# Optimization experiments

Measured on AMD Instinct MI355X. Metric: run time of the kernel, lower is better.

Reference implementation:

```python
import jax, jax.numpy as jnp
import numpy as np

B = 512        # events (graphs) in batch
NPE = 512      # nodes per event (structured so knn can be batched)
N = B * NPE    # total nodes = 262144
K = 6          # knn neighbors
F_IN = 128     # 2 * n_samples
H = 16         # conv1 out
OUT = 10       # graph_out
COORD_MAX = 16 # detector grid extent


def setup_inputs() -> dict:
    key = jax.random.key(0)
    k1, k2, k3, k4 = jax.random.split(key, 4)
    xy = jax.random.randint(k1, (N, 2), 0, COORD_MAX, dtype=jnp.int32)
    batch = jnp.repeat(jnp.arange(B, dtype=jnp.int32), NPE)  # coo[:,2] = event id
    coo = jnp.concatenate([xy, batch[:, None]], axis=1)       # [N,3] int
    x = jax.random.normal(k2, (N, F_IN), dtype=jnp.float32)
    W1 = jax.random.normal(k3, (F_IN, H), dtype=jnp.float32) * (1.0 / np.sqrt(F_IN))
    b1 = jnp.zeros((H,), dtype=jnp.float32)
    W2 = jax.random.normal(k4, (H, OUT), dtype=jnp.float32) * (1.0 / np.sqrt(H))
    b2 = jnp.zeros((OUT,), dtype=jnp.float32)
    return {"coo": coo, "x": x, "W1": W1, "b1": b1, "W2": W2, "b2": b2}


def knn_edges(coo):
    # knn_graph(coo, K, batch=coo[:,2], loop=False): batches are contiguous
    # blocks of NPE nodes, so reshape and do per-event brute-force knn.
    pos = coo.astype(jnp.float32).reshape(B, NPE, 3)
    # squared pairwise distances per event: [B, n, n]
    d = jnp.sum((pos[:, :, None, :] - pos[:, None, :, :]) ** 2, axis=-1)
    d = d + jnp.eye(NPE, dtype=d.dtype) * 1e9  # exclude self (loop=False)
    _, idx = jax.lax.top_k(-d, K)              # [B, n, K] neighbor indices (local)
    base = (jnp.arange(B, dtype=jnp.int32) * NPE)[:, None, None]
    src = (idx.astype(jnp.int32) + base).reshape(-1)                       # j (neighbor)
    dst = jnp.broadcast_to(jnp.arange(NPE, dtype=jnp.int32)[None, :, None] + base,
                           (B, NPE, K)).reshape(-1)                        # i (center)
    return src, dst


def gcn_conv(x, W, b, src, dst):
    # GCNConv: out = D^{-1/2} (A + I) D^{-1/2} X W + b
    loops = jnp.arange(N, dtype=jnp.int32)
    row = jnp.concatenate([dst, loops])  # target
    col = jnp.concatenate([src, loops])  # source
    deg = jax.ops.segment_sum(jnp.ones_like(row, dtype=x.dtype), row, num_segments=N)
    dinv = jnp.where(deg > 0, jax.lax.rsqrt(deg), 0.0)
    norm = dinv[row] * dinv[col]         # [E]
    h = x @ W                            # [N, F_out]
    msg = h[col] * norm[:, None]         # gather + scale
    return jax.ops.segment_sum(msg, row, num_segments=N) + b


def reference(coo, x, W1, b1, W2, b2):
    src, dst = knn_edges(coo)
    h = jax.nn.relu(gcn_conv(x, W1, b1, src, dst))
    out = gcn_conv(h, W2, b2, src, dst)  # [N, OUT] per-node output (n_lin == 0)
    return out
```

## Files before the change

### kernel.cpp

```cpp
#include <hip/hip_runtime.h>

#define NPE   512
#define F_IN  128
#define HDIM  16
#define ODIM  10

typedef __attribute__((ext_vector_type(8))) short short8;
typedef __attribute__((ext_vector_type(4))) float f32x4;

static __device__ __forceinline__ short f2bf(float f) {
  unsigned u = __builtin_bit_cast(unsigned, f);
  u = (u + 0x7fffu + ((u >> 16) & 1u)) >> 16;
  return (short)u;
}
static __device__ __forceinline__ float bflo(unsigned d) {
  return __builtin_bit_cast(float, d << 16);
}
static __device__ __forceinline__ float bfhi(unsigned d) {
  return __builtin_bit_cast(float, d & 0xffff0000u);
}
static __device__ __forceinline__ unsigned umin2(unsigned a, unsigned b) { return a < b ? a : b; }
static __device__ __forceinline__ unsigned umax2(unsigned a, unsigned b) { return a > b ? a : b; }

__global__ __launch_bounds__(512, 4) void gnet_fused(
    const int* __restrict__ coo, const float* __restrict__ x,
    const float* __restrict__ W1, const float* __restrict__ b1,
    const float* __restrict__ W2, const float* __restrict__ b2,
    float* __restrict__ out)
{
  __shared__ __align__(16) short    hbuf[NPE][24];
  __shared__ __align__(16) short    r_s [NPE][24];
  __shared__ unsigned       cnt_s [256];
  __shared__ unsigned       scan_s[256];
  __shared__ unsigned       cur_s [256];
  __shared__ unsigned       wtot_s[4];
  __shared__ unsigned short bucket_s[NPE];
  __shared__ unsigned       top7_s[256][8];
  __shared__ unsigned       tile_c;

  const int tid   = threadIdx.x;
  const int gbase = blockIdx.x * NPE;
  const int ln    = tid & 63;
  const int wv    = tid >> 6;
  const int lcol  = ln & 15;
  const int lkg   = ln >> 4;

  const int cx = coo[(gbase + tid) * 3 + 0];
  const int cy = coo[(gbase + tid) * 3 + 1];
  const int mycell = cy * 16 + cx;

  if (tid < 256) cnt_s[tid] = 0;
  if (tid == 0)  tile_c = 0;
  __syncthreads();
  atomicAdd(&cnt_s[mycell], 1u);
  __syncthreads();
  unsigned sv = 0;
  if (tid < 256) {
    sv = cnt_s[tid];
#pragma unroll
    for (int off = 1; off < 64; off <<= 1) {
      unsigned u = __shfl_up(sv, off, 64);
      if (ln >= off) sv += u;
    }
    if (ln == 63) wtot_s[wv] = sv;
  }
  __syncthreads();
  if (tid < 256) {
    unsigned add = 0;
#pragma unroll
    for (int w = 0; w < 3; ++w) if (w < wv) add += wtot_s[w];
    sv += add;
    scan_s[tid] = sv;
    cur_s[tid]  = sv - cnt_s[tid];
  }
  __syncthreads();
  {
    const unsigned slot = atomicAdd(&cur_s[mycell], 1u);
    bucket_s[slot] = (unsigned short)tid;
  }
  __syncthreads();

  short8 bw1[4];
#pragma unroll
  for (int s = 0; s < 4; ++s) {
#pragma unroll
    for (int e = 0; e < 8; ++e) {
      const int k = s * 32 + lkg * 8 + e;
      bw1[s][e] = f2bf(W1[k * HDIM + lcol]);
    }
  }

  if (tid < 256 && cnt_s[tid] != 0) {
    const int ccx = tid & 15, ccy = tid >> 4;
    unsigned k0 = 0x7fffffffu, k1 = k0, k2 = k0, k3 = k0, k4 = k0, k5 = k0, k6 = k0;
    auto insert7 = [&](unsigned key) {
      if (key < k6) {
        k6 = key;
        unsigned lo, hi;
        lo = umin2(k5, k6); hi = umax2(k5, k6); k5 = lo; k6 = hi;
        lo = umin2(k4, k5); hi = umax2(k4, k5); k4 = lo; k5 = hi;
        lo = umin2(k3, k4); hi = umax2(k3, k4); k3 = lo; k4 = hi;
        lo = umin2(k2, k3); hi = umax2(k2, k3); k2 = lo; k3 = hi;
        lo = umin2(k1, k2); hi = umax2(k1, k2); k1 = lo; k2 = hi;
        lo = umin2(k0, k1); hi = umax2(k0, k1); k0 = lo; k1 = hi;
      }
    };
    auto scan_cell = [&](int c, unsigned kb) {
      const unsigned e = scan_s[c];
      const unsigned n = cnt_s[c];
      for (unsigned q = e - n; q < e; ++q) insert7(kb | (unsigned)bucket_s[q]);
    };
    scan_cell(tid, 0u);
    for (int r = 1; r <= 15; ++r) {
      const unsigned r2 = (unsigned)(r * r);
      if (r2 > (k6 >> 9)) break;
      for (int sg = 0; sg < 2; ++sg) {
        const int yy = ccy + (sg ? r : -r);
        if (yy < 0 || yy > 15) continue;
        const int xlo = ccx - r < 0 ? 0 : ccx - r;
        const int xhi = ccx + r > 15 ? 15 : ccx + r;
        for (int xx = xlo; xx <= xhi; ++xx) {
          const int dx = xx - ccx;
          const unsigned kb = (unsigned)(dx * dx + (int)r2) << 9;
          if (kb < k6) scan_cell(yy * 16 + xx, kb);
        }
      }
      for (int sg = 0; sg < 2; ++sg) {
        const int xx = ccx + (sg ? r : -r);
        if (xx < 0 || xx > 15) continue;
        const int ylo = ccy - r + 1 < 0 ? 0 : ccy - r + 1;
        const int yhi = ccy + r - 1 > 15 ? 15 : ccy + r - 1;
        for (int yy = ylo; yy <= yhi; ++yy) {
          const int dy = yy - ccy;
          const unsigned kb = (unsigned)(dy * dy + (int)r2) << 9;
          if (kb < k6) scan_cell(yy * 16 + xx, kb);
        }
      }
    }
    unsigned* tp = top7_s[tid];
    tp[0] = k0; tp[1] = k1; tp[2] = k2; tp[3] = k3; tp[4] = k4; tp[5] = k5; tp[6] = k6;
  }

  for (;;) {
    int t = 0;
    if (ln == 0) t = (int)atomicAdd(&tile_c, 1u);
    t = __shfl(t, 0, 64);
    if (t >= 32) break;
    const int nt = t * 16;
    f32x4 acc = {0.f, 0.f, 0.f, 0.f};
#pragma unroll
    for (int s = 0; s < 4; ++s) {
      const float* xp = x + (size_t)(gbase + nt + lcol) * F_IN + s * 32 + lkg * 8;
      const float4 xa = *reinterpret_cast<const float4*>(xp);
      const float4 xb = *reinterpret_cast<const float4*>(xp + 4);
      short8 af;
      af[0] = f2bf(xa.x); af[1] = f2bf(xa.y); af[2] = f2bf(xa.z); af[3] = f2bf(xa.w);
      af[4] = f2bf(xb.x); af[5] = f2bf(xb.y); af[6] = f2bf(xb.z); af[7] = f2bf(xb.w);
      acc = __builtin_amdgcn_mfma_f32_16x16x32_bf16(af, bw1[s], acc, 0, 0, 0);
    }
#pragma unroll
    for (int i = 0; i < 4; ++i) {
      hbuf[nt + lkg * 4 + i][lcol] = f2bf(acc[i]);
    }
  }
  __syncthreads();

  const unsigned* tp = top7_s[mycell];
  const unsigned t0 = tp[0], t1 = tp[1], t2 = tp[2], t3 = tp[3];
  const unsigned t4 = tp[4], t5 = tp[5], t6 = tp[6];
  const unsigned selfkey = (unsigned)tid;
  int p = 7;
  p = (t6 == selfkey) ? 6 : p;
  p = (t5 == selfkey) ? 5 : p;
  p = (t4 == selfkey) ? 4 : p;
  p = (t3 == selfkey) ? 3 : p;
  p = (t2 == selfkey) ? 2 : p;
  p = (t1 == selfkey) ? 1 : p;
  p = (t0 == selfkey) ? 0 : p;
  const int nb0 = (int)((p > 0 ? t0 : t1) & 511u);
  const int nb1 = (int)((p > 1 ? t1 : t2) & 511u);
  const int nb2 = (int)((p > 2 ? t2 : t3) & 511u);
  const int nb3 = (int)((p > 3 ? t3 : t4) & 511u);
  const int nb4 = (int)((p > 4 ? t4 : t5) & 511u);
  const int nb5 = (int)((p > 5 ? t5 : t6) & 511u);

  {
    float acc[HDIM];
#pragma unroll
    for (int o = 0; o < HDIM; ++o) acc[o] = 0.f;
    const int rows[7] = {tid, nb0, nb1, nb2, nb3, nb4, nb5};
#pragma unroll
    for (int r = 0; r < 7; ++r) {
      const unsigned* hp = reinterpret_cast<const unsigned*>(hbuf[rows[r]]);
      const uint4 ha = *reinterpret_cast<const uint4*>(hp);
      const uint4 hb = *reinterpret_cast<const uint4*>(hp + 4);
      const unsigned hd[8] = {ha.x, ha.y, ha.z, ha.w, hb.x, hb.y, hb.z, hb.w};
#pragma unroll
      for (int q = 0; q < 8; ++q) {
        acc[2 * q]     += bflo(hd[q]);
        acc[2 * q + 1] += bfhi(hd[q]);
      }
    }
    const float inv = 1.0f / 7.0f;
    unsigned* rp = reinterpret_cast<unsigned*>(r_s[tid]);
#pragma unroll
    for (int q = 0; q < 8; ++q) {
      const float v0 = fmaxf(acc[2 * q]     * inv + b1[2 * q],     0.f);
      const float v1 = fmaxf(acc[2 * q + 1] * inv + b1[2 * q + 1], 0.f);
      rp[q] = (unsigned)(unsigned short)f2bf(v0) |
              ((unsigned)(unsigned short)f2bf(v1) << 16);
    }
  }
  __syncthreads();

  float* h2f = reinterpret_cast<float*>(hbuf);
  short8 bw2 = {0, 0, 0, 0, 0, 0, 0, 0};
  if (lkg < 2 && lcol < ODIM) {
#pragma unroll
    for (int e = 0; e < 8; ++e) {
      const int k = lkg * 8 + e;
      bw2[e] = f2bf(W2[k * ODIM + lcol]);
    }
  }
#pragma unroll
  for (int t = 0; t < 4; ++t) {
    const int nt = wv * 64 + t * 16;
    short8 af = {0, 0, 0, 0, 0, 0, 0, 0};
    if (lkg < 2) {
      af = *reinterpret_cast<const short8*>(&r_s[nt + lcol][lkg * 8]);
    }
    f32x4 acc = {0.f, 0.f, 0.f, 0.f};
    acc = __builtin_amdgcn_mfma_f32_16x16x32_bf16(af, bw2, acc, 0, 0, 0);
#pragma unroll
    for (int i = 0; i < 4; ++i) {
      if (lcol < ODIM) h2f[(nt + lkg * 4 + i) * 12 + lcol] = acc[i];
    }
  }
  __syncthreads();

  {
    float acc[ODIM];
#pragma unroll
    for (int c = 0; c < ODIM; ++c) acc[c] = 0.f;
    const int rows[7] = {tid, nb0, nb1, nb2, nb3, nb4, nb5};
#pragma unroll
    for (int r = 0; r < 7; ++r) {
      const float* hp = h2f + rows[r] * 12;
#pragma unroll
      for (int c = 0; c < ODIM; ++c) acc[c] += hp[c];
    }
    const float inv = 1.0f / 7.0f;
    float* op = out + (size_t)(gbase + tid) * ODIM;
#pragma unroll
    for (int c = 0; c < ODIM; c += 2) {
      float2 v;
      v.x = acc[c]     * inv + b2[c];
      v.y = acc[c + 1] * inv + b2[c + 1];
      *reinterpret_cast<float2*>(op + c) = v;
    }
  }
}

extern "C" void kernel_launch(void* const* d_in, const int* in_sizes, int n_in,
                              void* d_out, int out_size, void* d_ws, size_t ws_size,
                              hipStream_t stream) {
  const int*   coo = (const int*)  d_in[0];
  const float* x   = (const float*)d_in[1];
  const float* W1  = (const float*)d_in[2];
  const float* b1  = (const float*)d_in[3];
  const float* W2  = (const float*)d_in[4];
  const float* b2  = (const float*)d_in[5];
  gnet_fused<<<dim3(512), dim3(512), 0, stream>>>(coo, x, W1, b1, W2, b2,
                                                  (float*)d_out);
}
```

Measured before the change: 34.30 us.

## Overlap single-wave cell sort with GEMM tiles and vectorize bf16 packing

The cell counting sort now runs in wave 0 alone, without block-wide barriers. Waves 1-3 spin on a shared flag before the kNN search, and waves 4-7 go straight to the x·W1 MFMA tiles. The GEMM tiles now cover 32 rows each, with all global loads issued up front for more memory-level parallelism. bf16 conversion switches to the HIP packed intrinsics, and the final gather reads float4 vectors. The spin-wait without a barrier depends on LDS ordering through fences, and the wider tiles raise register pressure.

```diff
diff --git a/kernel.cpp b/kernel.cpp
--- a/kernel.cpp
+++ b/kernel.cpp
@@ -1,4 +1,5 @@
 #include <hip/hip_runtime.h>
+#include <hip/hip_bf16.h>
 
 #define NPE   512
 #define F_IN  128
@@ -8,10 +9,17 @@
 typedef __attribute__((ext_vector_type(8))) short short8;
 typedef __attribute__((ext_vector_type(4))) float f32x4;
 
+static __device__ __forceinline__ unsigned pkbf(float lo, float hi) {
+  __hip_bfloat162 h = __float22bfloat162_rn(make_float2(lo, hi));
+  unsigned r;
+  __builtin_memcpy(&r, &h, 4);
+  return r;
+}
 static __device__ __forceinline__ short f2bf(float f) {
-  unsigned u = __builtin_bit_cast(unsigned, f);
-  u = (u + 0x7fffu + ((u >> 16) & 1u)) >> 16;
-  return (short)u;
+  __hip_bfloat16 h = __float2bfloat16(f);
+  short r;
+  __builtin_memcpy(&r, &h, 2);
+  return r;
 }
 static __device__ __forceinline__ float bflo(unsigned d) {
   return __builtin_bit_cast(float, d << 16);
@@ -30,13 +38,14 @@
 {
   __shared__ __align__(16) short    hbuf[NPE][24];
   __shared__ __align__(16) short    r_s [NPE][24];
+  __shared__ unsigned short cellof_s[NPE];
   __shared__ unsigned       cnt_s [256];
   __shared__ unsigned       scan_s[256];
   __shared__ unsigned       cur_s [256];
-  __shared__ unsigned       wtot_s[4];
   __shared__ unsigned short bucket_s[NPE];
   __shared__ unsigned       top7_s[256][8];
   __shared__ unsigned       tile_c;
+  __shared__ unsigned       sortflag;
 
   const int tid   = threadIdx.x;
   const int gbase = blockIdx.x * NPE;
@@ -48,49 +57,58 @@
   const int cx = coo[(gbase + tid) * 3 + 0];
   const int cy = coo[(gbase + tid) * 3 + 1];
   const int mycell = cy * 16 + cx;
-
-  if (tid < 256) cnt_s[tid] = 0;
-  if (tid == 0)  tile_c = 0;
+  cellof_s[tid] = (unsigned short)mycell;
+  if (tid == 0) { tile_c = 0; sortflag = 0; }
   __syncthreads();
-  atomicAdd(&cnt_s[mycell], 1u);
-  __syncthreads();
-  unsigned sv = 0;
-  if (tid < 256) {
-    sv = cnt_s[tid];
+
+  short8 bw1[4];
+#pragma unroll
+  for (int s = 0; s < 4; ++s) {
+#pragma unroll
+    for (int e = 0; e < 8; ++e) {
+      const int k = s * 32 + lkg * 8 + e;
+      bw1[s][e] = f2bf(W1[k * HDIM + lcol]);
+    }
+  }
+
+  if (wv == 0) {
+#pragma unroll
+    for (int q = 0; q < 4; ++q) cnt_s[ln * 4 + q] = 0;
+    __threadfence_block();
+#pragma unroll
+    for (int q = 0; q < 8; ++q)
+      atomicAdd(&cnt_s[cellof_s[ln + q * 64]], 1u);
+    __threadfence_block();
+    const unsigned c0 = cnt_s[ln * 4 + 0], c1 = cnt_s[ln * 4 + 1];
+    const unsigned c2 = cnt_s[ln * 4 + 2], c3 = cnt_s[ln * 4 + 3];
+    const unsigned psum = c0 + c1 + c2 + c3;
+    unsigned sv = psum;
 #pragma unroll
     for (int off = 1; off < 64; off <<= 1) {
       unsigned u = __shfl_up(sv, off, 64);
       if (ln >= off) sv += u;
     }
-    if (ln == 63) wtot_s[wv] = sv;
-  }
-  __syncthreads();
-  if (tid < 256) {
-    unsigned add = 0;
-#pragma unroll
-    for (int w = 0; w < 3; ++w) if (w < wv) add += wtot_s[w];
-    sv += add;
-    scan_s[tid] = sv;
-    cur_s[tid]  = sv - cnt_s[tid];
-  }
-  __syncthreads();
-  {
-    const unsigned slot = atomicAdd(&cur_s[mycell], 1u);
-    bucket_s[slot] = (unsigned short)tid;
-  }
-  __syncthreads();
-
-  short8 bw1[4];
-#pragma unroll
-  for (int s = 0; s < 4; ++s) {
-#pragma unroll
-    for (int e = 0; e < 8; ++e) {
-      const int k = s * 32 + lkg * 8 + e;
-      bw1[s][e] = f2bf(W1[k * HDIM + lcol]);
-    }
-  }
-
-  if (tid < 256 && cnt_s[tid] != 0) {
+    const unsigned basex = sv - psum;
+    const unsigned e0 = basex + c0, e1 = e0 + c1, e2 = e1 + c2, e3 = e2 + c3;
+    scan_s[ln * 4 + 0] = e0; cur_s[ln * 4 + 0] = e0 - c0;
+    scan_s[ln * 4 + 1] = e1; cur_s[ln * 4 + 1] = e1 - c1;
+    scan_s[ln * 4 + 2] = e2; cur_s[ln * 4 + 2] = e2 - c2;
+    scan_s[ln * 4 + 3] = e3; cur_s[ln * 4 + 3] = e3 - c3;
+    __threadfence_block();
+#pragma unroll
+    for (int q = 0; q < 8; ++q) {
+      const int node = ln + q * 64;
+      const unsigned slot = atomicAdd(&cur_s[cellof_s[node]], 1u);
+      bucket_s[slot] = (unsigned short)node;
+    }
+    __threadfence_block();
+    if (ln == 0) *(volatile unsigned*)&sortflag = 1u;
+  } else if (wv < 4) {
+    while (*(volatile unsigned*)&sortflag == 0u) __builtin_amdgcn_s_sleep(8);
+    __threadfence_block();
+  }
+
+  if (wv < 4 && cnt_s[tid] != 0) {
     const int ccx = tid & 15, ccy = tid >> 4;
     unsigned k0 = 0x7fffffffu, k1 = k0, k2 = k0, k3 = k0, k4 = k0, k5 = k0, k6 = k0;
     auto insert7 = [&](unsigned key) {
@@ -145,22 +163,39 @@
     int t = 0;
     if (ln == 0) t = (int)atomicAdd(&tile_c, 1u);
     t = __shfl(t, 0, 64);
-    if (t >= 32) break;
-    const int nt = t * 16;
-    f32x4 acc = {0.f, 0.f, 0.f, 0.f};
+    if (t >= 16) break;
+    const int base = t * 32;
+    const float4* pA = reinterpret_cast<const float4*>(
+        x + (size_t)(gbase + base + lcol) * F_IN + lkg * 8);
+    const float4* pB = reinterpret_cast<const float4*>(
+        x + (size_t)(gbase + base + 16 + lcol) * F_IN + lkg * 8);
+    float4 a0 = pA[0],  a1 = pA[1],  a2 = pA[8],  a3 = pA[9];
+    float4 a4 = pA[16], a5 = pA[17], a6 = pA[24], a7 = pA[25];
+    float4 b0 = pB[0],  b1v = pB[1], b2v = pB[8], b3 = pB[9];
+    float4 b4 = pB[16], b5 = pB[17], b6 = pB[24], b7 = pB[25];
+
+    f32x4 accA = {0.f, 0.f, 0.f, 0.f};
+    f32x4 accB = {0.f, 0.f, 0.f, 0.f};
+    const float4 av[8] = {a0, a1, a2, a3, a4, a5, a6, a7};
+    const float4 bv[8] = {b0, b1v, b2v, b3, b4, b5, b6, b7};
 #pragma unroll
     for (int s = 0; s < 4; ++s) {
-      const float* xp = x + (size_t)(gbase + nt + lcol) * F_IN + s * 32 + lkg * 8;
-      const float4 xa = *reinterpret_cast<const float4*>(xp);
-      const float4 xb = *reinterpret_cast<const float4*>(xp + 4);
-      short8 af;
-      af[0] = f2bf(xa.x); af[1] = f2bf(xa.y); af[2] = f2bf(xa.z); af[3] = f2bf(xa.w);
-      af[4] = f2bf(xb.x); af[5] = f2bf(xb.y); af[6] = f2bf(xb.z); af[7] = f2bf(xb.w);
-      acc = __builtin_amdgcn_mfma_f32_16x16x32_bf16(af, bw1[s], acc, 0, 0, 0);
+      const float4 u = av[2 * s], v = av[2 * s + 1];
+      uint4 pk = {pkbf(u.x, u.y), pkbf(u.z, u.w), pkbf(v.x, v.y), pkbf(v.z, v.w)};
+      short8 af = __builtin_bit_cast(short8, pk);
+      accA = __builtin_amdgcn_mfma_f32_16x16x32_bf16(af, bw1[s], accA, 0, 0, 0);
+    }
+#pragma unroll
+    for (int s = 0; s < 4; ++s) {
+      const float4 u = bv[2 * s], v = bv[2 * s + 1];
+      uint4 pk = {pkbf(u.x, u.y), pkbf(u.z, u.w), pkbf(v.x, v.y), pkbf(v.z, v.w)};
+      short8 bf = __builtin_bit_cast(short8, pk);
+      accB = __builtin_amdgcn_mfma_f32_16x16x32_bf16(bf, bw1[s], accB, 0, 0, 0);
     }
 #pragma unroll
     for (int i = 0; i < 4; ++i) {
-      hbuf[nt + lkg * 4 + i][lcol] = f2bf(acc[i]);
+      hbuf[base + lkg * 4 + i][lcol]      = f2bf(accA[i]);
+      hbuf[base + 16 + lkg * 4 + i][lcol] = f2bf(accB[i]);
     }
   }
   __syncthreads();
@@ -207,8 +242,7 @@
     for (int q = 0; q < 8; ++q) {
       const float v0 = fmaxf(acc[2 * q]     * inv + b1[2 * q],     0.f);
       const float v1 = fmaxf(acc[2 * q + 1] * inv + b1[2 * q + 1], 0.f);
-      rp[q] = (unsigned)(unsigned short)f2bf(v0) |
-              ((unsigned)(unsigned short)f2bf(v1) << 16);
+      rp[q] = pkbf(v0, v1);
     }
   }
   __syncthreads();
@@ -239,17 +273,17 @@
   __syncthreads();
 
   {
-    float acc[ODIM];
-#pragma unroll
-    for (int c = 0; c < ODIM; ++c) acc[c] = 0.f;
+    f32x4 s0 = {0.f, 0.f, 0.f, 0.f}, s1 = s0, s2 = s0;
     const int rows[7] = {tid, nb0, nb1, nb2, nb3, nb4, nb5};
 #pragma unroll
     for (int r = 0; r < 7; ++r) {
-      const float* hp = h2f + rows[r] * 12;
-#pragma unroll
-      for (int c = 0; c < ODIM; ++c) acc[c] += hp[c];
+      const f32x4* hp = reinterpret_cast<const f32x4*>(h2f + rows[r] * 12);
+      s0 += hp[0]; s1 += hp[1]; s2 += hp[2];
     }
     const float inv = 1.0f / 7.0f;
+    float acc[12];
+#pragma unroll
+    for (int c = 0; c < 4; ++c) { acc[c] = s0[c]; acc[4 + c] = s1[c]; acc[8 + c] = s2[c]; }
     float* op = out + (size_t)(gbase + tid) * ODIM;
 #pragma unroll
     for (int c = 0; c < ODIM; c += 2) {
```

New measurement: 34.13 us. About the same (-0.5%).
